# Optimization experiments

Hardware: AMD Instinct MI355X
Metric: run time of the kernel (lower is better)

Reference implementation:

```python
import math
import jax, jax.numpy as jnp
import numpy as np

B, L, N, DM, H = 4, 12, 512, 64, 8
D = DM // H
FACTOR = 5  # args.spatial_factor


def setup_inputs() -> dict:
    key = jax.random.key(0)
    ks = jax.random.split(key, 6)
    s = 1.0 / math.sqrt(DM)
    return {
        "queries": jax.random.normal(ks[0], (B, L, N, DM), jnp.float32),
        "keys": jax.random.normal(ks[1], (B, L, N, DM), jnp.float32),
        "values": jax.random.normal(ks[2], (B, L, N, DM), jnp.float32),
        "Wq": jax.random.normal(ks[3], (DM, DM), jnp.float32) * s,
        "bq": jnp.zeros((DM,), jnp.float32),
        "Wk": jax.random.normal(ks[4], (DM, DM), jnp.float32) * s,
        "bk": jnp.zeros((DM,), jnp.float32),
        "Wv": jax.random.normal(ks[5], (DM, DM), jnp.float32) * s,
        "bv": jnp.zeros((DM,), jnp.float32),
    }


def reference(queries, keys, values, Wq, bq, Wk, bk, Wv, bv):
    # QKV projections (torch nn.Linear), then split heads and move to [B,H,N,L,D]
    q = jnp.transpose((queries @ Wq + bq).reshape(B, L, N, H, D), (0, 3, 2, 1, 4))
    k = jnp.transpose((keys @ Wk + bk).reshape(B, L, N, H, D), (0, 3, 2, 1, 4))
    v = jnp.transpose((values @ Wv + bv).reshape(B, L, N, H, D), (0, 3, 2, 1, 4))

    sample_k = min(FACTOR * int(np.ceil(np.log(N))), N)  # = n_top = effect_N

    # --- _prob_QK: random K sampling over the N (spatial) axis ---
    idx = jax.random.randint(jax.random.key(42), (N, sample_k), 0, N)  # [N, sk]
    K_sample = k[:, :, idx]                       # [B,H,N,sk,L,D] gather
    # Q.unsqueeze(-2) @ K_sample^T -> [B,H,N,L,sk], then transposed to [B,H,L,N,sk]
    qk_s = jnp.einsum('bhnld,bhnsld->bhlns', q, K_sample)
    M = qk_s.max(axis=-1) - qk_s.sum(axis=-1) / N  # sparsity measure [B,H,L,N]
    _, M_top = jax.lax.top_k(M, sample_k)          # [B,H,L,n_top]

    q_t = jnp.transpose(q, (0, 1, 3, 2, 4))        # [B,H,L,N,D]
    Q_red = jnp.take_along_axis(q_t, M_top[..., None], axis=3)  # [B,H,L,n_top,D]
    scores = jnp.einsum('bhltd,bhnld->bhltn', Q_red, k) / math.sqrt(D)

    # --- context: mean of V over nodes, overwritten at top queries ---
    attn = jax.nn.softmax(scores, axis=-1)                        # [B,H,L,n_top,N]
    attn_ret = jnp.einsum('bhltn,bhnld->bhltd', attn, v)          # [B,H,L,n_top,D]
    ctx = jnp.broadcast_to(v.mean(axis=2)[:, :, :, None, :], (B, H, L, N, D))
    bi = jnp.arange(B)[:, None, None, None]
    hi = jnp.arange(H)[None, :, None, None]
    li = jnp.arange(L)[None, None, :, None]
    ctx = ctx.at[bi, hi, li, M_top].set(attn_ret)                 # scatter-write

    out = jnp.transpose(ctx, (0, 2, 3, 1, 4)).reshape(B, L, N, DM)
    return out  # dropout p=0.0 -> identity
```

## Files before the change

kernel.cpp:

```cpp
#include <hip/hip_runtime.h>
#include <stdint.h>
#include <math.h>

#define BB 4
#define LL 12
#define NN 512
#define DMM 64
#define HH 8
#define DD 8
#define SK 35
#define IDX_TOTAL (NN*SK)
#define PADK 12

__device__ __forceinline__ void tf2x32(uint32_t k0, uint32_t k1, uint32_t x0, uint32_t x1,
                                       uint32_t& o0, uint32_t& o1) {
  const uint32_t ks2 = k0 ^ k1 ^ 0x1BD11BDAu;
  uint32_t a = x0 + k0, b = x1 + k1;
#define TF_R(r) { a += b; b = (b << (r)) | (b >> (32 - (r))); b ^= a; }
  TF_R(13) TF_R(15) TF_R(26) TF_R(6)
  a += k1;  b += ks2 + 1u;
  TF_R(17) TF_R(29) TF_R(16) TF_R(24)
  a += ks2; b += k0 + 2u;
  TF_R(13) TF_R(15) TF_R(26) TF_R(6)
  a += k0;  b += k1 + 3u;
  TF_R(17) TF_R(29) TF_R(16) TF_R(24)
  a += k1;  b += ks2 + 4u;
  TF_R(13) TF_R(15) TF_R(26) TF_R(6)
  a += ks2; b += k0 + 5u;
#undef TF_R
  o0 = a; o1 = b;
}

__global__ __launch_bounds__(256) void proj_idx_kernel(
    const float* __restrict__ Xq, const float* __restrict__ Xk, const float* __restrict__ Xv,
    const float* __restrict__ Wq_, const float* __restrict__ Wk_, const float* __restrict__ Wv_,
    const float* __restrict__ bq_, const float* __restrict__ bk_, const float* __restrict__ bv_,
    float* __restrict__ Oq, float* __restrict__ Ok, float* __restrict__ Ov,
    int* __restrict__ idxT) {
  const int tz = blockIdx.y;
  if (tz == 3) {
    int gid = blockIdx.x * 256 + threadIdx.x;
    if (gid < IDX_TOTAL) {
      int r = gid & (NN - 1);
      int s = gid >> 9;
      uint32_t ka, kb;
      tf2x32(0u, 42u, 0u, 1u, ka, kb);
      uint32_t b1, b2;
      tf2x32(ka, kb, 0u, (uint32_t)(r * SK + s), b1, b2);
      idxT[gid] = (int)((b1 ^ b2) & (uint32_t)(NN - 1));
    }
    return;
  }
  const float* X    = (tz == 0) ? Xq  : (tz == 1) ? Xk  : Xv;
  const float* W    = (tz == 0) ? Wq_ : (tz == 1) ? Wk_ : Wv_;
  const float* bias = (tz == 0) ? bq_ : (tz == 1) ? bk_ : bv_;
  float* O          = (tz == 0) ? Oq  : (tz == 1) ? Ok  : Ov;

  __shared__ __align__(16) float Ws[64][64];
  __shared__ __align__(16) float Xs[64][68];
  __shared__ float bs[64];

  const int tid = threadIdx.x;
  const size_t rowBase = (size_t)blockIdx.x * 64;
  const float* Xb = X + rowBase * 64;
  #pragma unroll
  for (int i = 0; i < 4; ++i) {
    int idx = tid + i*256;
    ((float4*)Ws)[idx] = ((const float4*)W)[idx];
    int r = idx >> 4, c = (idx & 15) << 2;
    *(float4*)&Xs[r][c] = ((const float4*)Xb)[idx];
  }
  if (tid < 64) bs[tid] = bias[tid];
  __syncthreads();

  const int hcol = tid & 7;
  const int rb   = tid >> 3;
  float4 bv0 = *(float4*)&bs[hcol*8];
  float4 bv1 = *(float4*)&bs[hcol*8+4];
  float acc[2][8];
  #pragma unroll
  for (int i = 0; i < 2; ++i) {
    acc[i][0]=bv0.x; acc[i][1]=bv0.y; acc[i][2]=bv0.z; acc[i][3]=bv0.w;
    acc[i][4]=bv1.x; acc[i][5]=bv1.y; acc[i][6]=bv1.z; acc[i][7]=bv1.w;
  }
  #pragma unroll 8
  for (int m = 0; m < 64; ++m) {
    float4 w0 = *(const float4*)&Ws[m][hcol*8];
    float4 w1 = *(const float4*)&Ws[m][hcol*8+4];
    float x0 = Xs[rb][m];
    float x1 = Xs[rb+32][m];
    acc[0][0]=fmaf(x0,w0.x,acc[0][0]); acc[0][1]=fmaf(x0,w0.y,acc[0][1]);
    acc[0][2]=fmaf(x0,w0.z,acc[0][2]); acc[0][3]=fmaf(x0,w0.w,acc[0][3]);
    acc[0][4]=fmaf(x0,w1.x,acc[0][4]); acc[0][5]=fmaf(x0,w1.y,acc[0][5]);
    acc[0][6]=fmaf(x0,w1.z,acc[0][6]); acc[0][7]=fmaf(x0,w1.w,acc[0][7]);
    acc[1][0]=fmaf(x1,w0.x,acc[1][0]); acc[1][1]=fmaf(x1,w0.y,acc[1][1]);
    acc[1][2]=fmaf(x1,w0.z,acc[1][2]); acc[1][3]=fmaf(x1,w0.w,acc[1][3]);
    acc[1][4]=fmaf(x1,w1.x,acc[1][4]); acc[1][5]=fmaf(x1,w1.y,acc[1][5]);
    acc[1][6]=fmaf(x1,w1.z,acc[1][6]); acc[1][7]=fmaf(x1,w1.w,acc[1][7]);
  }
  #pragma unroll
  for (int i = 0; i < 2; ++i) {
    size_t R = rowBase + rb + 32*i;
    int bI = (int)(R / (LL*NN));
    int lI = (int)((R / NN) % LL);
    int nI = (int)(R % NN);
    size_t off = ((((size_t)bI*HH + hcol)*LL + lI)*NN + nI)*DD;
    *(float4*)&O[off]     = make_float4(acc[i][0],acc[i][1],acc[i][2],acc[i][3]);
    *(float4*)&O[off + 4] = make_float4(acc[i][4],acc[i][5],acc[i][6],acc[i][7]);
  }
}

__global__ __launch_bounds__(512) void fused_kernel(
    const float* __restrict__ Qt, const float* __restrict__ Kt,
    const float* __restrict__ Vt, const int* __restrict__ idxT,
    float* __restrict__ out) {
  const int bid = blockIdx.x;
  const int l = bid % LL;
  const int h = (bid / LL) % HH;
  const int b = bid / (LL*HH);
  const int tid = threadIdx.x;
  const int wave = tid >> 6, lane = tid & 63;

  __shared__ __align__(16) float Ks[NN][PADK];
  __shared__ __align__(16) uint64_t keys[NN];
  __shared__ int sel[NN];
  __shared__ int topIdxL[SK + 1];
  __shared__ __align__(16) float attnOut[SK][8];
  __shared__ __align__(16) float redD[8][64][8];
  __shared__ __align__(16) float vm[8];

  const size_t slabOff = (size_t)bid * (NN*DD);

  {
    const float4* kg = (const float4*)(Kt + slabOff);
    float4 a = kg[tid*2], c = kg[tid*2+1];
    *(float4*)&Ks[tid][0] = a; *(float4*)&Ks[tid][4] = c;
  }
  const float4* qp = (const float4*)(Qt + slabOff + (size_t)tid*DD);
  float4 qa = qp[0], qb = qp[1];
  int jv[SK];
  const int* gi = idxT + tid;
  #pragma unroll
  for (int s = 0; s < SK; ++s) jv[s] = gi[s*NN];
  sel[tid] = -1;
  __syncthreads();

  {
    float mx = -INFINITY, sm = 0.f;
    #pragma unroll
    for (int s = 0; s < SK; ++s) {
      int j = jv[s];
      float4 c0 = *(const float4*)&Ks[j][0];
      float4 c1 = *(const float4*)&Ks[j][4];
      float dot = qa.x*c0.x + qa.y*c0.y + qa.z*c0.z + qa.w*c0.w
                + qb.x*c1.x + qb.y*c1.y + qb.z*c1.z + qb.w*c1.w;
      mx = fmaxf(mx, dot);
      sm += dot;
    }
    float m = mx - sm * (1.0f/NN);
    uint32_t u = __float_as_uint(m);
    uint32_t fk = (u & 0x80000000u) ? ~u : (u | 0x80000000u);
    keys[tid] = ((uint64_t)fk << 32) | (uint32_t)(NN - 1 - tid);
  }
  __syncthreads();

  {
    const uint64_t my = keys[tid];
    const ulonglong2* kq = (const ulonglong2*)keys;
    int cnt = 0;
    #pragma unroll 8
    for (int jb = 0; jb < NN/2; ++jb) {
      ulonglong2 kv = kq[jb];
      cnt += (kv.x > my) ? 1 : 0;
      cnt += (kv.y > my) ? 1 : 0;
    }
    if (cnt < SK) { topIdxL[cnt] = tid; sel[tid] = cnt; }
  }
  __syncthreads();

  const float4* kp = (const float4*)(Kt + slabOff);
  const float4* vp = (const float4*)(Vt + slabOff);

  if (wave == 0) {
    float a[8] = {0,0,0,0,0,0,0,0};
    #pragma unroll
    for (int j = 0; j < 8; ++j) {
      const float4* vr = vp + (size_t)(lane + 64*j)*2;
      float4 v0 = vr[0], v1 = vr[1];
      a[0]+=v0.x; a[1]+=v0.y; a[2]+=v0.z; a[3]+=v0.w;
      a[4]+=v1.x; a[5]+=v1.y; a[6]+=v1.z; a[7]+=v1.w;
    }
    *(float4*)&redD[0][lane][0] = make_float4(a[0],a[1],a[2],a[3]);
    *(float4*)&redD[0][lane][4] = make_float4(a[4],a[5],a[6],a[7]);
    const int d = lane & 7, g = lane >> 3;
    float s = 0.f;
    #pragma unroll
    for (int k = 0; k < 8; ++k) s += redD[0][g*8+k][d];
    s += __shfl_xor(s, 8); s += __shfl_xor(s, 16); s += __shfl_xor(s, 32);
    if (lane < 8) vm[lane] = s * (1.0f/NN);
  } else {
    const int base = (wave - 1) * 5;
    auto do_rows = [&](int t1, int t2, bool has2) {
      const int n1 = topIdxL[t1];
      const int n2 = has2 ? topIdxL[t2] : n1;
      const float4* q1p = (const float4*)(Qt + slabOff + (size_t)n1*DD);
      const float4* q2p = (const float4*)(Qt + slabOff + (size_t)n2*DD);
      float4 q1a = q1p[0], q1b = q1p[1];
      float4 q2a = q2p[0], q2b = q2p[1];
      float p1[8], p2[8];
      float mx1 = -INFINITY, mx2 = -INFINITY;
      #pragma unroll
      for (int j = 0; j < 8; ++j) {
        int key = lane + 64*j;
        float4 ca = kp[key*2], cb = kp[key*2+1];
        float s1 = q1a.x*ca.x + q1a.y*ca.y + q1a.z*ca.z + q1a.w*ca.w
                 + q1b.x*cb.x + q1b.y*cb.y + q1b.z*cb.z + q1b.w*cb.w;
        float s2 = q2a.x*ca.x + q2a.y*ca.y + q2a.z*ca.z + q2a.w*ca.w
                 + q2b.x*cb.x + q2b.y*cb.y + q2b.z*cb.z + q2b.w*cb.w;
        s1 *= 0.35355339059327373f;
        s2 *= 0.35355339059327373f;
        p1[j] = s1; p2[j] = s2;
        mx1 = fmaxf(mx1, s1); mx2 = fmaxf(mx2, s2);
      }
      #pragma unroll
      for (int off = 32; off >= 1; off >>= 1) {
        mx1 = fmaxf(mx1, __shfl_xor(mx1, off));
        mx2 = fmaxf(mx2, __shfl_xor(mx2, off));
      }
      float sum1 = 0.f, sum2 = 0.f;
      #pragma unroll
      for (int j = 0; j < 8; ++j) {
        p1[j] = __expf(p1[j] - mx1); sum1 += p1[j];
        p2[j] = __expf(p2[j] - mx2); sum2 += p2[j];
      }
      #pragma unroll
      for (int off = 32; off >= 1; off >>= 1) {
        sum1 += __shfl_xor(sum1, off);
        sum2 += __shfl_xor(sum2, off);
      }
      float a1[8] = {0,0,0,0,0,0,0,0}, a2[8] = {0,0,0,0,0,0,0,0};
      #pragma unroll
      for (int j = 0; j < 8; ++j) {
        int key = lane + 64*j;
        float4 va = vp[key*2], vb = vp[key*2+1];
        float w1 = p1[j], w2 = p2[j];
        a1[0]=fmaf(w1,va.x,a1[0]); a1[1]=fmaf(w1,va.y,a1[1]);
        a1[2]=fmaf(w1,va.z,a1[2]); a1[3]=fmaf(w1,va.w,a1[3]);
        a1[4]=fmaf(w1,vb.x,a1[4]); a1[5]=fmaf(w1,vb.y,a1[5]);
        a1[6]=fmaf(w1,vb.z,a1[6]); a1[7]=fmaf(w1,vb.w,a1[7]);
        a2[0]=fmaf(w2,va.x,a2[0]); a2[1]=fmaf(w2,va.y,a2[1]);
        a2[2]=fmaf(w2,va.z,a2[2]); a2[3]=fmaf(w2,va.w,a2[3]);
        a2[4]=fmaf(w2,vb.x,a2[4]); a2[5]=fmaf(w2,vb.y,a2[5]);
        a2[6]=fmaf(w2,vb.z,a2[6]); a2[7]=fmaf(w2,vb.w,a2[7]);
      }
      const int d = lane & 7, g = lane >> 3;
      {
        *(float4*)&redD[wave][lane][0] = make_float4(a1[0],a1[1],a1[2],a1[3]);
        *(float4*)&redD[wave][lane][4] = make_float4(a1[4],a1[5],a1[6],a1[7]);
        float s = 0.f;
        #pragma unroll
        for (int k = 0; k < 8; ++k) s += redD[wave][g*8+k][d];
        s += __shfl_xor(s, 8); s += __shfl_xor(s, 16); s += __shfl_xor(s, 32);
        if (lane < 8) attnOut[t1][lane] = s * (1.0f / sum1);
      }
      if (has2) {
        *(float4*)&redD[wave][lane][0] = make_float4(a2[0],a2[1],a2[2],a2[3]);
        *(float4*)&redD[wave][lane][4] = make_float4(a2[4],a2[5],a2[6],a2[7]);
        float s = 0.f;
        #pragma unroll
        for (int k = 0; k < 8; ++k) s += redD[wave][g*8+k][d];
        s += __shfl_xor(s, 8); s += __shfl_xor(s, 16); s += __shfl_xor(s, 32);
        if (lane < 8) attnOut[t2][lane] = s * (1.0f / sum2);
      }
    };
    do_rows(base, base + 1, true);
    do_rows(base + 2, base + 3, true);
    do_rows(base + 4, base + 4, false);
  }
  __syncthreads();

  {
    int t = sel[tid];
    float4 o0, o1;
    if (t >= 0) { o0 = *(const float4*)&attnOut[t][0]; o1 = *(const float4*)&attnOut[t][4]; }
    else        { o0 = *(const float4*)&vm[0];         o1 = *(const float4*)&vm[4]; }
    float* ob = out + ((size_t)(b*LL + l)*NN + tid)*DMM + h*DD;
    *(float4*)&ob[0] = o0;
    *(float4*)&ob[4] = o1;
  }
}

extern "C" void kernel_launch(void* const* d_in, const int* in_sizes, int n_in,
                              void* d_out, int out_size, void* d_ws, size_t ws_size,
                              hipStream_t stream) {
  const float* q  = (const float*)d_in[0];
  const float* k  = (const float*)d_in[1];
  const float* v  = (const float*)d_in[2];
  const float* Wq = (const float*)d_in[3];
  const float* bq = (const float*)d_in[4];
  const float* Wk = (const float*)d_in[5];
  const float* bk = (const float*)d_in[6];
  const float* Wv = (const float*)d_in[7];
  const float* bv = (const float*)d_in[8];
  float* out = (float*)d_out;

  const size_t slab = (size_t)BB*HH*LL*NN*DD;
  float* qT = (float*)d_ws;
  float* kT = qT + slab;
  float* vT = kT + slab;
  int*   idxT = (int*)(vT + slab);

  proj_idx_kernel<<<dim3((BB*LL*NN)/64, 4), 256, 0, stream>>>(
      q, k, v, Wq, Wk, Wv, bq, bk, bv, qT, kT, vT, idxT);
  fused_kernel<<<BB*HH*LL, 512, 0, stream>>>(qT, kT, vT, idxT, out);
}
```

Before: 60.79 us.

## Split fused attention into sparsity-key and half-slab attention kernels

Splits the single per-(b,h,l) fused kernel into two launches, each using two 256-thread blocks per slab. The first computes the sparsity measure keys and writes them to workspace. The second ranks the full key set, handles only the top-k rows that fall in its half, and writes its half of the output. This doubles the block count for better GPU occupancy and spreads the attention rows across all waves, at the cost of an extra launch, a global round trip for the keys, and duplicated ranking and V-mean work in both halves.

```diff
diff --git a/kernel.cpp b/kernel.cpp
--- a/kernel.cpp
+++ b/kernel.cpp
@@ -110,62 +110,83 @@
   }
 }
 
-__global__ __launch_bounds__(512) void fused_kernel(
+__global__ __launch_bounds__(256) void mkeys_kernel(
     const float* __restrict__ Qt, const float* __restrict__ Kt,
-    const float* __restrict__ Vt, const int* __restrict__ idxT,
+    const int* __restrict__ idxT, uint32_t* __restrict__ fkW) {
+  const int gb = blockIdx.x;
+  const int bid = gb >> 1, half = gb & 1;
+  const int tid = threadIdx.x;
+  __shared__ __align__(16) float Ks[NN][PADK];
+  const size_t slabOff = (size_t)bid * (NN*DD);
+
+  const float4* kg = (const float4*)(Kt + slabOff);
+  #pragma unroll
+  for (int i = 0; i < 2; ++i) {
+    int r = tid + i*256;
+    float4 a = kg[r*2], c = kg[r*2+1];
+    *(float4*)&Ks[r][0] = a; *(float4*)&Ks[r][4] = c;
+  }
+  const int row = half*256 + tid;
+  const float4* qp = (const float4*)(Qt + slabOff + (size_t)row*DD);
+  float4 qa = qp[0], qb = qp[1];
+  int jv[SK];
+  const int* gi = idxT + row;
+  #pragma unroll
+  for (int s = 0; s < SK; ++s) jv[s] = gi[s*NN];
+  __syncthreads();
+
+  float mx = -INFINITY, sm = 0.f;
+  #pragma unroll
+  for (int s = 0; s < SK; ++s) {
+    int j = jv[s];
+    float4 c0 = *(const float4*)&Ks[j][0];
+    float4 c1 = *(const float4*)&Ks[j][4];
+    float dot = qa.x*c0.x + qa.y*c0.y + qa.z*c0.z + qa.w*c0.w
+              + qb.x*c1.x + qb.y*c1.y + qb.z*c1.z + qb.w*c1.w;
+    mx = fmaxf(mx, dot);
+    sm += dot;
+  }
+  float m = mx - sm * (1.0f/NN);
+  uint32_t u = __float_as_uint(m);
+  fkW[bid*NN + row] = (u & 0x80000000u) ? ~u : (u | 0x80000000u);
+}
+
+__global__ __launch_bounds__(256) void attn2_kernel(
+    const float* __restrict__ Qt, const float* __restrict__ Kt,
+    const float* __restrict__ Vt, const uint32_t* __restrict__ fkW,
     float* __restrict__ out) {
-  const int bid = blockIdx.x;
+  const int gb = blockIdx.x;
+  const int bid = gb >> 1, half = gb & 1;
   const int l = bid % LL;
   const int h = (bid / LL) % HH;
   const int b = bid / (LL*HH);
   const int tid = threadIdx.x;
   const int wave = tid >> 6, lane = tid & 63;
 
-  __shared__ __align__(16) float Ks[NN][PADK];
   __shared__ __align__(16) uint64_t keys[NN];
-  __shared__ int sel[NN];
-  __shared__ int topIdxL[SK + 1];
+  __shared__ int sel[256];
+  __shared__ int listRow[SK];
+  __shared__ int listSlot[SK];
+  __shared__ int cnt2;
   __shared__ __align__(16) float attnOut[SK][8];
-  __shared__ __align__(16) float redD[8][64][8];
+  __shared__ __align__(16) float redD[4][64][8];
   __shared__ __align__(16) float vm[8];
 
   const size_t slabOff = (size_t)bid * (NN*DD);
 
   {
-    const float4* kg = (const float4*)(Kt + slabOff);
-    float4 a = kg[tid*2], c = kg[tid*2+1];
-    *(float4*)&Ks[tid][0] = a; *(float4*)&Ks[tid][4] = c;
-  }
-  const float4* qp = (const float4*)(Qt + slabOff + (size_t)tid*DD);
-  float4 qa = qp[0], qb = qp[1];
-  int jv[SK];
-  const int* gi = idxT + tid;
-  #pragma unroll
-  for (int s = 0; s < SK; ++s) jv[s] = gi[s*NN];
+    const uint32_t* fp = fkW + bid*NN;
+    uint32_t f0 = fp[tid], f1 = fp[tid + 256];
+    keys[tid]       = ((uint64_t)f0 << 32) | (uint32_t)(NN - 1 - tid);
+    keys[tid + 256] = ((uint64_t)f1 << 32) | (uint32_t)(NN - 1 - (tid + 256));
+  }
   sel[tid] = -1;
+  if (tid == 0) cnt2 = 0;
   __syncthreads();
 
   {
-    float mx = -INFINITY, sm = 0.f;
-    #pragma unroll
-    for (int s = 0; s < SK; ++s) {
-      int j = jv[s];
-      float4 c0 = *(const float4*)&Ks[j][0];
-      float4 c1 = *(const float4*)&Ks[j][4];
-      float dot = qa.x*c0.x + qa.y*c0.y + qa.z*c0.z + qa.w*c0.w
-                + qb.x*c1.x + qb.y*c1.y + qb.z*c1.z + qb.w*c1.w;
-      mx = fmaxf(mx, dot);
-      sm += dot;
-    }
-    float m = mx - sm * (1.0f/NN);
-    uint32_t u = __float_as_uint(m);
-    uint32_t fk = (u & 0x80000000u) ? ~u : (u | 0x80000000u);
-    keys[tid] = ((uint64_t)fk << 32) | (uint32_t)(NN - 1 - tid);
-  }
-  __syncthreads();
-
-  {
-    const uint64_t my = keys[tid];
+    const int row = half*256 + tid;
+    const uint64_t my = keys[row];
     const ulonglong2* kq = (const ulonglong2*)keys;
     int cnt = 0;
     #pragma unroll 8
@@ -174,9 +195,15 @@
       cnt += (kv.x > my) ? 1 : 0;
       cnt += (kv.y > my) ? 1 : 0;
     }
-    if (cnt < SK) { topIdxL[cnt] = tid; sel[tid] = cnt; }
-  }
-  __syncthreads();
+    if (cnt < SK) {
+      sel[tid] = cnt;
+      int p = atomicAdd(&cnt2, 1);
+      listRow[p] = row;
+      listSlot[p] = cnt;
+    }
+  }
+  __syncthreads();
+  const int C = cnt2;
 
   const float4* kp = (const float4*)(Kt + slabOff);
   const float4* vp = (const float4*)(Vt + slabOff);
@@ -198,85 +225,85 @@
     for (int k = 0; k < 8; ++k) s += redD[0][g*8+k][d];
     s += __shfl_xor(s, 8); s += __shfl_xor(s, 16); s += __shfl_xor(s, 32);
     if (lane < 8) vm[lane] = s * (1.0f/NN);
-  } else {
-    const int base = (wave - 1) * 5;
-    auto do_rows = [&](int t1, int t2, bool has2) {
-      const int n1 = topIdxL[t1];
-      const int n2 = has2 ? topIdxL[t2] : n1;
-      const float4* q1p = (const float4*)(Qt + slabOff + (size_t)n1*DD);
-      const float4* q2p = (const float4*)(Qt + slabOff + (size_t)n2*DD);
-      float4 q1a = q1p[0], q1b = q1p[1];
-      float4 q2a = q2p[0], q2b = q2p[1];
-      float p1[8], p2[8];
-      float mx1 = -INFINITY, mx2 = -INFINITY;
+  }
+
+  auto do_rows = [&](int t1, int t2, bool has2) {
+    const int n1 = listRow[t1];
+    const int n2 = has2 ? listRow[t2] : n1;
+    const int s1o = listSlot[t1];
+    const int s2o = has2 ? listSlot[t2] : s1o;
+    const float4* q1p = (const float4*)(Qt + slabOff + (size_t)n1*DD);
+    const float4* q2p = (const float4*)(Qt + slabOff + (size_t)n2*DD);
+    float4 q1a = q1p[0], q1b = q1p[1];
+    float4 q2a = q2p[0], q2b = q2p[1];
+    float p1[8], p2[8];
+    float mx1 = -INFINITY, mx2 = -INFINITY;
+    #pragma unroll
+    for (int j = 0; j < 8; ++j) {
+      int key = lane + 64*j;
+      float4 ca = kp[key*2], cb = kp[key*2+1];
+      float s1 = q1a.x*ca.x + q1a.y*ca.y + q1a.z*ca.z + q1a.w*ca.w
+               + q1b.x*cb.x + q1b.y*cb.y + q1b.z*cb.z + q1b.w*cb.w;
+      float s2 = q2a.x*ca.x + q2a.y*ca.y + q2a.z*ca.z + q2a.w*ca.w
+               + q2b.x*cb.x + q2b.y*cb.y + q2b.z*cb.z + q2b.w*cb.w;
+      s1 *= 0.35355339059327373f;
+      s2 *= 0.35355339059327373f;
+      p1[j] = s1; p2[j] = s2;
+      mx1 = fmaxf(mx1, s1); mx2 = fmaxf(mx2, s2);
+    }
+    #pragma unroll
+    for (int off = 32; off >= 1; off >>= 1) {
+      mx1 = fmaxf(mx1, __shfl_xor(mx1, off));
+      mx2 = fmaxf(mx2, __shfl_xor(mx2, off));
+    }
+    float sum1 = 0.f, sum2 = 0.f;
+    #pragma unroll
+    for (int j = 0; j < 8; ++j) {
+      p1[j] = __expf(p1[j] - mx1); sum1 += p1[j];
+      p2[j] = __expf(p2[j] - mx2); sum2 += p2[j];
+    }
+    #pragma unroll
+    for (int off = 32; off >= 1; off >>= 1) {
+      sum1 += __shfl_xor(sum1, off);
+      sum2 += __shfl_xor(sum2, off);
+    }
+    float a1[8] = {0,0,0,0,0,0,0,0}, a2[8] = {0,0,0,0,0,0,0,0};
+    #pragma unroll
+    for (int j = 0; j < 8; ++j) {
+      int key = lane + 64*j;
+      float4 va = vp[key*2], vb = vp[key*2+1];
+      float w1 = p1[j], w2 = p2[j];
+      a1[0]=fmaf(w1,va.x,a1[0]); a1[1]=fmaf(w1,va.y,a1[1]);
+      a1[2]=fmaf(w1,va.z,a1[2]); a1[3]=fmaf(w1,va.w,a1[3]);
+      a1[4]=fmaf(w1,vb.x,a1[4]); a1[5]=fmaf(w1,vb.y,a1[5]);
+      a1[6]=fmaf(w1,vb.z,a1[6]); a1[7]=fmaf(w1,vb.w,a1[7]);
+      a2[0]=fmaf(w2,va.x,a2[0]); a2[1]=fmaf(w2,va.y,a2[1]);
+      a2[2]=fmaf(w2,va.z,a2[2]); a2[3]=fmaf(w2,va.w,a2[3]);
+      a2[4]=fmaf(w2,vb.x,a2[4]); a2[5]=fmaf(w2,vb.y,a2[5]);
+      a2[6]=fmaf(w2,vb.z,a2[6]); a2[7]=fmaf(w2,vb.w,a2[7]);
+    }
+    const int d = lane & 7, g = lane >> 3;
+    {
+      *(float4*)&redD[wave][lane][0] = make_float4(a1[0],a1[1],a1[2],a1[3]);
+      *(float4*)&redD[wave][lane][4] = make_float4(a1[4],a1[5],a1[6],a1[7]);
+      float s = 0.f;
       #pragma unroll
-      for (int j = 0; j < 8; ++j) {
-        int key = lane + 64*j;
-        float4 ca = kp[key*2], cb = kp[key*2+1];
-        float s1 = q1a.x*ca.x + q1a.y*ca.y + q1a.z*ca.z + q1a.w*ca.w
-                 + q1b.x*cb.x + q1b.y*cb.y + q1b.z*cb.z + q1b.w*cb.w;
-        float s2 = q2a.x*ca.x + q2a.y*ca.y + q2a.z*ca.z + q2a.w*ca.w
-                 + q2b.x*cb.x + q2b.y*cb.y + q2b.z*cb.z + q2b.w*cb.w;
-        s1 *= 0.35355339059327373f;
-        s2 *= 0.35355339059327373f;
-        p1[j] = s1; p2[j] = s2;
-        mx1 = fmaxf(mx1, s1); mx2 = fmaxf(mx2, s2);
-      }
+      for (int k = 0; k < 8; ++k) s += redD[wave][g*8+k][d];
+      s += __shfl_xor(s, 8); s += __shfl_xor(s, 16); s += __shfl_xor(s, 32);
+      if (lane < 8) attnOut[s1o][lane] = s * (1.0f / sum1);
+    }
+    if (has2) {
+      *(float4*)&redD[wave][lane][0] = make_float4(a2[0],a2[1],a2[2],a2[3]);
+      *(float4*)&redD[wave][lane][4] = make_float4(a2[4],a2[5],a2[6],a2[7]);
+      float s = 0.f;
       #pragma unroll
-      for (int off = 32; off >= 1; off >>= 1) {
-        mx1 = fmaxf(mx1, __shfl_xor(mx1, off));
-        mx2 = fmaxf(mx2, __shfl_xor(mx2, off));
-      }
-      float sum1 = 0.f, sum2 = 0.f;
-      #pragma unroll
-      for (int j = 0; j < 8; ++j) {
-        p1[j] = __expf(p1[j] - mx1); sum1 += p1[j];
-        p2[j] = __expf(p2[j] - mx2); sum2 += p2[j];
-      }
-      #pragma unroll
-      for (int off = 32; off >= 1; off >>= 1) {
-        sum1 += __shfl_xor(sum1, off);
-        sum2 += __shfl_xor(sum2, off);
-      }
-      float a1[8] = {0,0,0,0,0,0,0,0}, a2[8] = {0,0,0,0,0,0,0,0};
-      #pragma unroll
-      for (int j = 0; j < 8; ++j) {
-        int key = lane + 64*j;
-        float4 va = vp[key*2], vb = vp[key*2+1];
-        float w1 = p1[j], w2 = p2[j];
-        a1[0]=fmaf(w1,va.x,a1[0]); a1[1]=fmaf(w1,va.y,a1[1]);
-        a1[2]=fmaf(w1,va.z,a1[2]); a1[3]=fmaf(w1,va.w,a1[3]);
-        a1[4]=fmaf(w1,vb.x,a1[4]); a1[5]=fmaf(w1,vb.y,a1[5]);
-        a1[6]=fmaf(w1,vb.z,a1[6]); a1[7]=fmaf(w1,vb.w,a1[7]);
-        a2[0]=fmaf(w2,va.x,a2[0]); a2[1]=fmaf(w2,va.y,a2[1]);
-        a2[2]=fmaf(w2,va.z,a2[2]); a2[3]=fmaf(w2,va.w,a2[3]);
-        a2[4]=fmaf(w2,vb.x,a2[4]); a2[5]=fmaf(w2,vb.y,a2[5]);
-        a2[6]=fmaf(w2,vb.z,a2[6]); a2[7]=fmaf(w2,vb.w,a2[7]);
-      }
-      const int d = lane & 7, g = lane >> 3;
-      {
-        *(float4*)&redD[wave][lane][0] = make_float4(a1[0],a1[1],a1[2],a1[3]);
-        *(float4*)&redD[wave][lane][4] = make_float4(a1[4],a1[5],a1[6],a1[7]);
-        float s = 0.f;
-        #pragma unroll
-        for (int k = 0; k < 8; ++k) s += redD[wave][g*8+k][d];
-        s += __shfl_xor(s, 8); s += __shfl_xor(s, 16); s += __shfl_xor(s, 32);
-        if (lane < 8) attnOut[t1][lane] = s * (1.0f / sum1);
-      }
-      if (has2) {
-        *(float4*)&redD[wave][lane][0] = make_float4(a2[0],a2[1],a2[2],a2[3]);
-        *(float4*)&redD[wave][lane][4] = make_float4(a2[4],a2[5],a2[6],a2[7]);
-        float s = 0.f;
-        #pragma unroll
-        for (int k = 0; k < 8; ++k) s += redD[wave][g*8+k][d];
-        s += __shfl_xor(s, 8); s += __shfl_xor(s, 16); s += __shfl_xor(s, 32);
-        if (lane < 8) attnOut[t2][lane] = s * (1.0f / sum2);
-      }
-    };
-    do_rows(base, base + 1, true);
-    do_rows(base + 2, base + 3, true);
-    do_rows(base + 4, base + 4, false);
-  }
+      for (int k = 0; k < 8; ++k) s += redD[wave][g*8+k][d];
+      s += __shfl_xor(s, 8); s += __shfl_xor(s, 16); s += __shfl_xor(s, 32);
+      if (lane < 8) attnOut[s2o][lane] = s * (1.0f / sum2);
+    }
+  };
+  for (int it = wave*2; it < C; it += 8)
+    do_rows(it, it + 1, (it + 1) < C);
   __syncthreads();
 
   {
@@ -284,7 +311,8 @@
     float4 o0, o1;
     if (t >= 0) { o0 = *(const float4*)&attnOut[t][0]; o1 = *(const float4*)&attnOut[t][4]; }
     else        { o0 = *(const float4*)&vm[0];         o1 = *(const float4*)&vm[4]; }
-    float* ob = out + ((size_t)(b*LL + l)*NN + tid)*DMM + h*DD;
+    const int n = half*256 + tid;
+    float* ob = out + ((size_t)(b*LL + l)*NN + n)*DMM + h*DD;
     *(float4*)&ob[0] = o0;
     *(float4*)&ob[4] = o1;
   }
@@ -309,8 +337,10 @@
   float* kT = qT + slab;
   float* vT = kT + slab;
   int*   idxT = (int*)(vT + slab);
+  uint32_t* fkW = (uint32_t*)(idxT + IDX_TOTAL);
 
   proj_idx_kernel<<<dim3((BB*LL*NN)/64, 4), 256, 0, stream>>>(
       q, k, v, Wq, Wk, Wv, bq, bk, bv, qT, kT, vT, idxT);
-  fused_kernel<<<BB*HH*LL, 512, 0, stream>>>(qT, kT, vT, idxT, out);
-}
+  mkeys_kernel<<<BB*HH*LL*2, 256, 0, stream>>>(qT, kT, idxT, fkW);
+  attn2_kernel<<<BB*HH*LL*2, 256, 0, stream>>>(qT, kT, vT, fkW, out);
+}
```

After: 61.22 us. Within noise of the previous version (+0.7%).

## Stage V in LDS, split rank counting across thread groups, read K/V from shared memory

Applied to the files above, without the earlier changes.

The top-k rank count now has each thread compare four keys against a 128-key slice, with partial counts summed through shared memory. This keeps the total number of comparisons the same but gives each thread more independent work. V is loaded into LDS once, with its global load issued before the barrier so it overlaps the ranking. The attention and mean loops then read K and V from LDS instead of re-reading global memory. The cost is about 30KB of extra shared memory per block, which may lower occupancy.

```diff
diff --git a/kernel.cpp b/kernel.cpp
--- a/kernel.cpp
+++ b/kernel.cpp
@@ -122,7 +122,9 @@
   const int wave = tid >> 6, lane = tid & 63;
 
   __shared__ __align__(16) float Ks[NN][PADK];
+  __shared__ __align__(16) float Vs[NN][PADK];
   __shared__ __align__(16) uint64_t keys[NN];
+  __shared__ __align__(16) int partial[NN][4];
   __shared__ int sel[NN];
   __shared__ int topIdxL[SK + 1];
   __shared__ __align__(16) float attnOut[SK][8];
@@ -165,30 +167,45 @@
   __syncthreads();
 
   {
-    const uint64_t my = keys[tid];
-    const ulonglong2* kq = (const ulonglong2*)keys;
-    int cnt = 0;
+    const int qgrp = tid >> 7, li = tid & 127;
+    uint64_t k0 = keys[li], k1 = keys[li+128], k2 = keys[li+256], k3 = keys[li+384];
+    const ulonglong2* kq = (const ulonglong2*)(keys + qgrp*128);
+    int c0 = 0, c1 = 0, c2 = 0, c3 = 0;
     #pragma unroll 8
-    for (int jb = 0; jb < NN/2; ++jb) {
+    for (int jb = 0; jb < 64; ++jb) {
       ulonglong2 kv = kq[jb];
-      cnt += (kv.x > my) ? 1 : 0;
-      cnt += (kv.y > my) ? 1 : 0;
+      c0 += (kv.x > k0) ? 1 : 0; c0 += (kv.y > k0) ? 1 : 0;
+      c1 += (kv.x > k1) ? 1 : 0; c1 += (kv.y > k1) ? 1 : 0;
+      c2 += (kv.x > k2) ? 1 : 0; c2 += (kv.y > k2) ? 1 : 0;
+      c3 += (kv.x > k3) ? 1 : 0; c3 += (kv.y > k3) ? 1 : 0;
     }
+    partial[li][qgrp]     = c0;
+    partial[li+128][qgrp] = c1;
+    partial[li+256][qgrp] = c2;
+    partial[li+384][qgrp] = c3;
+  }
+  const float4* vg = (const float4*)(Vt + slabOff) + tid*2;
+  float4 v0 = vg[0], v1 = vg[1];
+  __syncthreads();
+
+  {
+    int4 pc = *(const int4*)&partial[tid][0];
+    int cnt = pc.x + pc.y + pc.z + pc.w;
     if (cnt < SK) { topIdxL[cnt] = tid; sel[tid] = cnt; }
   }
-  __syncthreads();
-
-  const float4* kp = (const float4*)(Kt + slabOff);
-  const float4* vp = (const float4*)(Vt + slabOff);
+  *(float4*)&Vs[tid][0] = v0;
+  *(float4*)&Vs[tid][4] = v1;
+  __syncthreads();
 
   if (wave == 0) {
     float a[8] = {0,0,0,0,0,0,0,0};
     #pragma unroll
     for (int j = 0; j < 8; ++j) {
-      const float4* vr = vp + (size_t)(lane + 64*j)*2;
-      float4 v0 = vr[0], v1 = vr[1];
-      a[0]+=v0.x; a[1]+=v0.y; a[2]+=v0.z; a[3]+=v0.w;
-      a[4]+=v1.x; a[5]+=v1.y; a[6]+=v1.z; a[7]+=v1.w;
+      int n = lane + 64*j;
+      float4 w0 = *(const float4*)&Vs[n][0];
+      float4 w1 = *(const float4*)&Vs[n][4];
+      a[0]+=w0.x; a[1]+=w0.y; a[2]+=w0.z; a[3]+=w0.w;
+      a[4]+=w1.x; a[5]+=w1.y; a[6]+=w1.z; a[7]+=w1.w;
     }
     *(float4*)&redD[0][lane][0] = make_float4(a[0],a[1],a[2],a[3]);
     *(float4*)&redD[0][lane][4] = make_float4(a[4],a[5],a[6],a[7]);
@@ -211,8 +228,9 @@
       float mx1 = -INFINITY, mx2 = -INFINITY;
       #pragma unroll
       for (int j = 0; j < 8; ++j) {
-        int key = lane + 64*j;
-        float4 ca = kp[key*2], cb = kp[key*2+1];
+        int n = lane + 64*j;
+        float4 ca = *(const float4*)&Ks[n][0];
+        float4 cb = *(const float4*)&Ks[n][4];
         float s1 = q1a.x*ca.x + q1a.y*ca.y + q1a.z*ca.z + q1a.w*ca.w
                  + q1b.x*cb.x + q1b.y*cb.y + q1b.z*cb.z + q1b.w*cb.w;
         float s2 = q2a.x*ca.x + q2a.y*ca.y + q2a.z*ca.z + q2a.w*ca.w
@@ -241,8 +259,9 @@
       float a1[8] = {0,0,0,0,0,0,0,0}, a2[8] = {0,0,0,0,0,0,0,0};
       #pragma unroll
       for (int j = 0; j < 8; ++j) {
-        int key = lane + 64*j;
-        float4 va = vp[key*2], vb = vp[key*2+1];
+        int n = lane + 64*j;
+        float4 va = *(const float4*)&Vs[n][0];
+        float4 vb = *(const float4*)&Vs[n][4];
         float w1 = p1[j], w2 = p2[j];
         a1[0]=fmaf(w1,va.x,a1[0]); a1[1]=fmaf(w1,va.y,a1[1]);
         a1[2]=fmaf(w1,va.z,a1[2]); a1[3]=fmaf(w1,va.w,a1[3]);
```

Result: faster. 57.15 us (-6.0%).
